# Kernel tuning notes

Measured on AMD Instinct MI355X. Metric: run time of the kernel, lower is better.

The kernel has to match this reference:

```python
import jax, jax.numpy as jnp
import numpy as np

B = 2048      # batchsize from init_kwargs
TAU = 0.5     # temperature from init_kwargs
EPS = 1e-8    # torch CosineSimilarity eps


def _neg_idx(b):
    # For each row i of the (2B,2B) similarity matrix, the columns that are
    # negatives: everything except the diagonal (i) and the positive partner
    # ((i+B) mod 2B). Matches torch mask 1-(eye(k=B)+eye(k=-B)+eye()).
    n = 2 * b
    rows = np.arange(n)
    partner = (rows + b) % n
    cols = np.tile(np.arange(n), (n, 1))
    mask = (cols != rows[:, None]) & (cols != partner[:, None])
    return cols[mask].reshape(n, n - 2)


NEG_IDX = jnp.asarray(_neg_idx(B))  # (2B, 2B-2), int


def setup_inputs() -> dict:
    key = jax.random.key(0)
    k1, k2 = jax.random.split(key)
    D = 1024
    return {
        "z_orig": jax.random.normal(k1, (B, D), dtype=jnp.float32),
        "z_augment": jax.random.normal(k2, (B, D), dtype=jnp.float32),
    }


def reference(z_orig, z_augment):
    n = 2 * B
    z = jnp.concatenate([z_augment, z_orig], axis=0)            # (2B, D)
    norms = jnp.linalg.norm(z, axis=-1, keepdims=True)
    zn = z / jnp.maximum(norms, EPS)
    sim = zn @ zn.T                                             # (2B, 2B) cosine sims
    idx = jnp.arange(n)
    pos = sim[idx, (idx + B) % n]                               # (2B,) positive pairs
    neg = jnp.take_along_axis(sim, NEG_IDX, axis=1)             # (2B, 2B-2)
    logits = jnp.concatenate([pos[:, None], neg], axis=1) / TAU # (2B, 2B-1)
    # CrossEntropy with label 0, reduction='sum':
    loss = jnp.sum(jax.nn.logsumexp(logits, axis=1) - logits[:, 0])
    return loss / n
```

## Files before the change

kernel.cpp:

```cpp
#include <hip/hip_runtime.h>
#include <hip/hip_bf16.h>
#include <math.h>


#define BB   2048
#define N2   4096
#define DIM  1024
#define TAUI 2.0f
#define EPSN 1e-8f

#define BM  128
#define BN  128
#define BKK 64
#define NP  64
#define NBLK 528

typedef __attribute__((ext_vector_type(4))) float f32x4;
typedef __attribute__((ext_vector_type(8))) short s16x8;

__device__ __forceinline__ void gll16(const void* g, void* l) {
    __builtin_amdgcn_global_load_lds(
        (const __attribute__((address_space(1))) void*)g,
        (__attribute__((address_space(3))) void*)l, 16, 0, 0);
}

__global__ __launch_bounds__(256) void k_prep(const float* __restrict__ zO,
                                              const float* __restrict__ zA,
                                              __hip_bfloat16* __restrict__ zb) {
    int row = blockIdx.x;
    const float* zr = (row < BB) ? (zA + (size_t)row * DIM)
                                 : (zO + (size_t)(row - BB) * DIM);
    int t = threadIdx.x;
    float4 v = *(const float4*)(zr + t * 4);
    float s = v.x * v.x + v.y * v.y + v.z * v.z + v.w * v.w;
    for (int m = 1; m < 64; m <<= 1) s += __shfl_xor(s, m);
    __shared__ float wsum[4];
    __shared__ float inv_s;
    int wv = t >> 6, ln = t & 63;
    if (ln == 0) wsum[wv] = s;
    __syncthreads();
    if (t == 0)
        inv_s = 1.0f / fmaxf(sqrtf(wsum[0] + wsum[1] + wsum[2] + wsum[3]), EPSN);
    __syncthreads();
    float inv = inv_s;
    __hip_bfloat16 h0 = __float2bfloat16(v.x * inv);
    __hip_bfloat16 h1 = __float2bfloat16(v.y * inv);
    __hip_bfloat16 h2 = __float2bfloat16(v.z * inv);
    __hip_bfloat16 h3 = __float2bfloat16(v.w * inv);
    ushort4 o;
    o.x = *(unsigned short*)&h0;
    o.y = *(unsigned short*)&h1;
    o.z = *(unsigned short*)&h2;
    o.w = *(unsigned short*)&h3;
    ((ushort4*)zb)[(size_t)row * (DIM / 4) + t] = o;
}

__global__ __launch_bounds__(256) void k_lse(const __hip_bfloat16* __restrict__ zb,
                                             float* __restrict__ pm,
                                             float* __restrict__ pl,
                                             float* __restrict__ pos) {
    __shared__ __hip_bfloat16 As[BM * BKK];
    __shared__ __hip_bfloat16 Bs[BN * BKK];

    int lin = blockIdx.x;
    int ti = (int)((65.0f - sqrtf(4225.0f - 8.0f * (float)lin)) * 0.5f);
    while ((ti + 1) * (65 - (ti + 1)) / 2 <= lin) ti++;
    while (ti * (65 - ti) / 2 > lin) ti--;
    int tj = ti + (lin - ti * (65 - ti) / 2);

    int ibase = ti * BM, jbase = tj * BN;
    int tid = threadIdx.x;
    int w = tid >> 6, l = tid & 63;
    int wr = w >> 1, wc = w & 1;
    int rl = l & 15, kg = l >> 4;

    const __hip_bfloat16* Ag = zb + (size_t)ibase * DIM;
    const __hip_bfloat16* Bg = zb + (size_t)jbase * DIM;

    f32x4 acc[4][4];
#pragma unroll
    for (int m = 0; m < 4; m++)
#pragma unroll
        for (int n = 0; n < 4; n++) acc[m][n] = (f32x4){0.f, 0.f, 0.f, 0.f};

    int srow = l >> 3;
    int scol = (l & 7) * 8;

    for (int kt = 0; kt < DIM; kt += BKK) {
        __syncthreads();
#pragma unroll
        for (int s4 = 0; s4 < 4; s4++) {
            int s = w * 4 + s4;
            int grow = 8 * s + srow;
            gll16(Ag + (size_t)grow * DIM + kt + scol, &As[s * 512]);
            gll16(Bg + (size_t)grow * DIM + kt + scol, &Bs[s * 512]);
        }
        __syncthreads();

#pragma unroll
        for (int kk = 0; kk < 2; kk++) {
            s16x8 a[4], b[4];
#pragma unroll
            for (int m = 0; m < 4; m++)
                a[m] = *(const s16x8*)&As[(wr * 64 + m * 16 + rl) * BKK + kk * 32 + kg * 8];
#pragma unroll
            for (int n = 0; n < 4; n++)
                b[n] = *(const s16x8*)&Bs[(wc * 64 + n * 16 + rl) * BKK + kk * 32 + kg * 8];
#pragma unroll
            for (int m = 0; m < 4; m++)
#pragma unroll
                for (int n = 0; n < 4; n++)
                    acc[m][n] = __builtin_amdgcn_mfma_f32_16x16x32_bf16(
                        a[m], b[n], acc[m][n], 0, 0, 0);
        }
    }

    int rowbase = ibase + wr * 64;
    int colbase = jbase + wc * 64;
    int slot = tj * 2 + wc;
#pragma unroll
    for (int m = 0; m < 4; m++) {
#pragma unroll
        for (int r = 0; r < 4; r++) {
            int ig = rowbase + m * 16 + kg * 4 + r;
            int pp = (ig + BB) & (N2 - 1);
            float v[4];
            float rmax = -1e30f;
#pragma unroll
            for (int n = 0; n < 4; n++) {
                int jg = colbase + n * 16 + rl;
                float val = acc[m][n][r] * TAUI;
                if (jg == pp) { pos[ig] = val; pos[jg] = val; }
                if (jg == ig) val = -1e30f;
                v[n] = val;
                rmax = fmaxf(rmax, val);
            }
#pragma unroll
            for (int mk = 1; mk < 16; mk <<= 1)
                rmax = fmaxf(rmax, __shfl_xor(rmax, mk));
            float ssum = 0.f;
#pragma unroll
            for (int n = 0; n < 4; n++) ssum += __expf(v[n] - rmax);
#pragma unroll
            for (int mk = 1; mk < 16; mk <<= 1) ssum += __shfl_xor(ssum, mk);
            if (rl == 0) {
                pm[(size_t)ig * NP + slot] = rmax;
                pl[(size_t)ig * NP + slot] = ssum;
            }
        }
    }

    if (ti != tj) {
        int slot2 = ti * 2 + wr;
#pragma unroll
        for (int n = 0; n < 4; n++) {
            float cmax = -1e30f;
#pragma unroll
            for (int m = 0; m < 4; m++)
#pragma unroll
                for (int r = 0; r < 4; r++)
                    cmax = fmaxf(cmax, acc[m][n][r] * TAUI);
            cmax = fmaxf(cmax, __shfl_xor(cmax, 16));
            cmax = fmaxf(cmax, __shfl_xor(cmax, 32));
            float cs = 0.f;
#pragma unroll
            for (int m = 0; m < 4; m++)
#pragma unroll
                for (int r = 0; r < 4; r++)
                    cs += __expf(acc[m][n][r] * TAUI - cmax);
            cs += __shfl_xor(cs, 16);
            cs += __shfl_xor(cs, 32);
            if (l < 16) {
                int jg = colbase + n * 16 + rl;
                pm[(size_t)jg * NP + slot2] = cmax;
                pl[(size_t)jg * NP + slot2] = cs;
            }
        }
    }
}

__global__ __launch_bounds__(256) void k_combine(const float* __restrict__ pm,
                                                 const float* __restrict__ pl,
                                                 const float* __restrict__ pos,
                                                 float* __restrict__ out) {
    int row = blockIdx.x * 256 + threadIdx.x;
    const float* P = pm + (size_t)row * NP;
    const float* L = pl + (size_t)row * NP;
    float M = -1e30f;
#pragma unroll
    for (int c = 0; c < NP; c++) M = fmaxf(M, P[c]);
    float S = 0.f;
#pragma unroll
    for (int c = 0; c < NP; c++) S += L[c] * __expf(P[c] - M);
    float v = M + __logf(S) - pos[row];
    for (int mk = 1; mk < 64; mk <<= 1) v += __shfl_xor(v, mk);
    __shared__ float wsum[4];
    int wv = threadIdx.x >> 6, ln = threadIdx.x & 63;
    if (ln == 0) wsum[wv] = v;
    __syncthreads();
    if (threadIdx.x == 0)
        atomicAdd(out, (wsum[0] + wsum[1] + wsum[2] + wsum[3]) * (1.0f / (float)N2));
}

extern "C" void kernel_launch(void* const* d_in, const int* in_sizes, int n_in,
                              void* d_out, int out_size, void* d_ws, size_t ws_size,
                              hipStream_t stream) {
    const float* zO = (const float*)d_in[0];
    const float* zA = (const float*)d_in[1];
    float* out = (float*)d_out;

    __hip_bfloat16* zb = (__hip_bfloat16*)d_ws;
    float* pm  = (float*)((char*)d_ws + (size_t)N2 * DIM * 2);
    float* pl  = pm + (size_t)N2 * NP;
    float* pos = pl + (size_t)N2 * NP;

    hipMemsetAsync(out, 0, sizeof(float), stream);
    k_prep<<<N2, 256, 0, stream>>>(zO, zA, zb);
    k_lse<<<NBLK, 256, 0, stream>>>(zb, pm, pl, pos);
    k_combine<<<N2 / 256, 256, 0, stream>>>(pm, pl, pos, out);
}
```

Before: 133.8 us.

## Double-buffer LDS tiles in the similarity GEMM to overlap loads with MFMA

Turns the shared-memory A/B tiles in the fused GEMM+logsumexp kernel into two buffers. The next K-slice is prefetched with global_load_lds while MFMAs run on the current one, and explicit vmcnt/lgkmcnt waits plus raw barriers order the work. The goal is to hide global load latency that the old load-sync-compute loop exposed. In exchange it doubles LDS use, which may lower occupancy, and it depends on a hand-counted vmcnt value.

```diff
diff --git a/kernel.cpp b/kernel.cpp
--- a/kernel.cpp
+++ b/kernel.cpp
@@ -12,6 +12,7 @@
 #define BM  128
 #define BN  128
 #define BKK 64
+#define NK  (DIM / BKK)
 #define NP  64
 #define NBLK 528
 
@@ -59,8 +60,8 @@
                                              float* __restrict__ pm,
                                              float* __restrict__ pl,
                                              float* __restrict__ pos) {
-    __shared__ __hip_bfloat16 As[BM * BKK];
-    __shared__ __hip_bfloat16 Bs[BN * BKK];
+    __shared__ __hip_bfloat16 As[2][BM * BKK];
+    __shared__ __hip_bfloat16 Bs[2][BN * BKK];
 
     int lin = blockIdx.x;
     int ti = (int)((65.0f - sqrtf(4225.0f - 8.0f * (float)lin)) * 0.5f);
@@ -86,26 +87,37 @@
     int srow = l >> 3;
     int scol = (l & 7) * 8;
 
-    for (int kt = 0; kt < DIM; kt += BKK) {
-        __syncthreads();
+    auto stage = [&](int buf, int kt) {
 #pragma unroll
         for (int s4 = 0; s4 < 4; s4++) {
             int s = w * 4 + s4;
             int grow = 8 * s + srow;
-            gll16(Ag + (size_t)grow * DIM + kt + scol, &As[s * 512]);
-            gll16(Bg + (size_t)grow * DIM + kt + scol, &Bs[s * 512]);
-        }
-        __syncthreads();
+            gll16(Ag + (size_t)grow * DIM + kt + scol, &As[buf][s * 512]);
+            gll16(Bg + (size_t)grow * DIM + kt + scol, &Bs[buf][s * 512]);
+        }
+    };
+
+    stage(0, 0);
+    int cur = 0;
+    for (int kt = 0; kt < NK; kt++) {
+        if (kt + 1 < NK) {
+            stage(cur ^ 1, (kt + 1) * BKK);
+            asm volatile("s_waitcnt vmcnt(8)" ::: "memory");
+        } else {
+            asm volatile("s_waitcnt vmcnt(0)" ::: "memory");
+        }
+        __builtin_amdgcn_sched_barrier(0);
+        __builtin_amdgcn_s_barrier();
 
 #pragma unroll
         for (int kk = 0; kk < 2; kk++) {
             s16x8 a[4], b[4];
 #pragma unroll
             for (int m = 0; m < 4; m++)
-                a[m] = *(const s16x8*)&As[(wr * 64 + m * 16 + rl) * BKK + kk * 32 + kg * 8];
+                a[m] = *(const s16x8*)&As[cur][(wr * 64 + m * 16 + rl) * BKK + kk * 32 + kg * 8];
 #pragma unroll
             for (int n = 0; n < 4; n++)
-                b[n] = *(const s16x8*)&Bs[(wc * 64 + n * 16 + rl) * BKK + kk * 32 + kg * 8];
+                b[n] = *(const s16x8*)&Bs[cur][(wc * 64 + n * 16 + rl) * BKK + kk * 32 + kg * 8];
 #pragma unroll
             for (int m = 0; m < 4; m++)
 #pragma unroll
@@ -113,6 +125,11 @@
                     acc[m][n] = __builtin_amdgcn_mfma_f32_16x16x32_bf16(
                         a[m], b[n], acc[m][n], 0, 0, 0);
         }
+
+        asm volatile("s_waitcnt lgkmcnt(0)" ::: "memory");
+        __builtin_amdgcn_sched_barrier(0);
+        __builtin_amdgcn_s_barrier();
+        cur ^= 1;
     }
 
     int rowbase = ibase + wr * 64;
```

Result: no change. 133.8 us (+0.0%).

## Swizzle LDS tiles, use 8 waves per GEMM tile, streamline prep and combine

Applied to the files above, without the earlier changes.

The LSE GEMM kernel now runs 512 threads (a 2x4 wave grid, each wave computing 64x32) instead of 256, which halves the per-wave accumulators. It also applies an XOR swizzle to the LDS chunk layout during global-to-LDS loads and MFMA operand reads, to avoid LDS bank conflicts. The partial-result slot count grows to 128, and the buffer is zeroed with a memset so unused slots are harmless. The prep kernel now handles one row per wave with no block barriers, and the combine kernel uses vectorized loads with an online max/sum. The costs are an extra memset and twice the partial storage.

```diff
diff --git a/kernel.cpp b/kernel.cpp
--- a/kernel.cpp
+++ b/kernel.cpp
@@ -12,8 +12,9 @@
 #define BM  128
 #define BN  128
 #define BKK 64
-#define NP  64
-#define NBLK 528
+#define NK  (DIM / BKK)
+#define NP  128
+#define NTRI 528
 
 typedef __attribute__((ext_vector_type(4))) float f32x4;
 typedef __attribute__((ext_vector_type(8))) short s16x8;
@@ -27,35 +28,36 @@
 __global__ __launch_bounds__(256) void k_prep(const float* __restrict__ zO,
                                               const float* __restrict__ zA,
                                               __hip_bfloat16* __restrict__ zb) {
-    int row = blockIdx.x;
+    int row = (blockIdx.x * 256 + threadIdx.x) >> 6;
+    int lane = threadIdx.x & 63;
     const float* zr = (row < BB) ? (zA + (size_t)row * DIM)
                                  : (zO + (size_t)(row - BB) * DIM);
-    int t = threadIdx.x;
-    float4 v = *(const float4*)(zr + t * 4);
-    float s = v.x * v.x + v.y * v.y + v.z * v.z + v.w * v.w;
+    float4 v[4];
+    float s = 0.f;
+#pragma unroll
+    for (int q = 0; q < 4; q++) {
+        v[q] = *(const float4*)(zr + q * 256 + lane * 4);
+        s += v[q].x * v[q].x + v[q].y * v[q].y + v[q].z * v[q].z + v[q].w * v[q].w;
+    }
+#pragma unroll
     for (int m = 1; m < 64; m <<= 1) s += __shfl_xor(s, m);
-    __shared__ float wsum[4];
-    __shared__ float inv_s;
-    int wv = t >> 6, ln = t & 63;
-    if (ln == 0) wsum[wv] = s;
-    __syncthreads();
-    if (t == 0)
-        inv_s = 1.0f / fmaxf(sqrtf(wsum[0] + wsum[1] + wsum[2] + wsum[3]), EPSN);
-    __syncthreads();
-    float inv = inv_s;
-    __hip_bfloat16 h0 = __float2bfloat16(v.x * inv);
-    __hip_bfloat16 h1 = __float2bfloat16(v.y * inv);
-    __hip_bfloat16 h2 = __float2bfloat16(v.z * inv);
-    __hip_bfloat16 h3 = __float2bfloat16(v.w * inv);
-    ushort4 o;
-    o.x = *(unsigned short*)&h0;
-    o.y = *(unsigned short*)&h1;
-    o.z = *(unsigned short*)&h2;
-    o.w = *(unsigned short*)&h3;
-    ((ushort4*)zb)[(size_t)row * (DIM / 4) + t] = o;
-}
-
-__global__ __launch_bounds__(256) void k_lse(const __hip_bfloat16* __restrict__ zb,
+    float inv = 1.0f / fmaxf(sqrtf(s), EPSN);
+#pragma unroll
+    for (int q = 0; q < 4; q++) {
+        __hip_bfloat16 h0 = __float2bfloat16(v[q].x * inv);
+        __hip_bfloat16 h1 = __float2bfloat16(v[q].y * inv);
+        __hip_bfloat16 h2 = __float2bfloat16(v[q].z * inv);
+        __hip_bfloat16 h3 = __float2bfloat16(v[q].w * inv);
+        ushort4 o;
+        o.x = *(unsigned short*)&h0;
+        o.y = *(unsigned short*)&h1;
+        o.z = *(unsigned short*)&h2;
+        o.w = *(unsigned short*)&h3;
+        ((ushort4*)zb)[(size_t)row * 256 + q * 64 + lane] = o;
+    }
+}
+
+__global__ __launch_bounds__(512) void k_lse(const __hip_bfloat16* __restrict__ zb,
                                              float* __restrict__ pm,
                                              float* __restrict__ pl,
                                              float* __restrict__ pos) {
@@ -71,26 +73,26 @@
     int ibase = ti * BM, jbase = tj * BN;
     int tid = threadIdx.x;
     int w = tid >> 6, l = tid & 63;
-    int wr = w >> 1, wc = w & 1;
+    int wr = w >> 2, wc = w & 3;
     int rl = l & 15, kg = l >> 4;
+    int cx = l & 7;
+    int srow = l >> 3;
+    int scol = ((cx ^ srow) * 8);
 
     const __hip_bfloat16* Ag = zb + (size_t)ibase * DIM;
     const __hip_bfloat16* Bg = zb + (size_t)jbase * DIM;
 
-    f32x4 acc[4][4];
+    f32x4 acc[4][2];
 #pragma unroll
     for (int m = 0; m < 4; m++)
 #pragma unroll
-        for (int n = 0; n < 4; n++) acc[m][n] = (f32x4){0.f, 0.f, 0.f, 0.f};
-
-    int srow = l >> 3;
-    int scol = (l & 7) * 8;
+        for (int n = 0; n < 2; n++) acc[m][n] = (f32x4){0.f, 0.f, 0.f, 0.f};
 
     for (int kt = 0; kt < DIM; kt += BKK) {
         __syncthreads();
 #pragma unroll
-        for (int s4 = 0; s4 < 4; s4++) {
-            int s = w * 4 + s4;
+        for (int s4 = 0; s4 < 2; s4++) {
+            int s = w * 2 + s4;
             int grow = 8 * s + srow;
             gll16(Ag + (size_t)grow * DIM + kt + scol, &As[s * 512]);
             gll16(Bg + (size_t)grow * DIM + kt + scol, &Bs[s * 512]);
@@ -99,35 +101,36 @@
 
 #pragma unroll
         for (int kk = 0; kk < 2; kk++) {
-            s16x8 a[4], b[4];
-#pragma unroll
-            for (int m = 0; m < 4; m++)
-                a[m] = *(const s16x8*)&As[(wr * 64 + m * 16 + rl) * BKK + kk * 32 + kg * 8];
-#pragma unroll
-            for (int n = 0; n < 4; n++)
-                b[n] = *(const s16x8*)&Bs[(wc * 64 + n * 16 + rl) * BKK + kk * 32 + kg * 8];
-#pragma unroll
-            for (int m = 0; m < 4; m++)
-#pragma unroll
-                for (int n = 0; n < 4; n++)
+            s16x8 a[4], b[2];
+            int ch = (((kk * 4 + kg) ^ (rl & 7)) * 8);
+#pragma unroll
+            for (int m = 0; m < 4; m++)
+                a[m] = *(const s16x8*)&As[(wr * 64 + m * 16 + rl) * BKK + ch];
+#pragma unroll
+            for (int n = 0; n < 2; n++)
+                b[n] = *(const s16x8*)&Bs[(wc * 32 + n * 16 + rl) * BKK + ch];
+#pragma unroll
+            for (int m = 0; m < 4; m++)
+#pragma unroll
+                for (int n = 0; n < 2; n++)
                     acc[m][n] = __builtin_amdgcn_mfma_f32_16x16x32_bf16(
                         a[m], b[n], acc[m][n], 0, 0, 0);
         }
     }
 
     int rowbase = ibase + wr * 64;
-    int colbase = jbase + wc * 64;
-    int slot = tj * 2 + wc;
+    int colbase = jbase + wc * 32;
+    int slot = tj * 4 + wc;
 #pragma unroll
     for (int m = 0; m < 4; m++) {
 #pragma unroll
         for (int r = 0; r < 4; r++) {
             int ig = rowbase + m * 16 + kg * 4 + r;
             int pp = (ig + BB) & (N2 - 1);
-            float v[4];
+            float v[2];
             float rmax = -1e30f;
 #pragma unroll
-            for (int n = 0; n < 4; n++) {
+            for (int n = 0; n < 2; n++) {
                 int jg = colbase + n * 16 + rl;
                 float val = acc[m][n][r] * TAUI;
                 if (jg == pp) { pos[ig] = val; pos[jg] = val; }
@@ -140,7 +143,7 @@
                 rmax = fmaxf(rmax, __shfl_xor(rmax, mk));
             float ssum = 0.f;
 #pragma unroll
-            for (int n = 0; n < 4; n++) ssum += __expf(v[n] - rmax);
+            for (int n = 0; n < 2; n++) ssum += __expf(v[n] - rmax);
 #pragma unroll
             for (int mk = 1; mk < 16; mk <<= 1) ssum += __shfl_xor(ssum, mk);
             if (rl == 0) {
@@ -153,7 +156,7 @@
     if (ti != tj) {
         int slot2 = ti * 2 + wr;
 #pragma unroll
-        for (int n = 0; n < 4; n++) {
+        for (int n = 0; n < 2; n++) {
             float cmax = -1e30f;
 #pragma unroll
             for (int m = 0; m < 4; m++)
@@ -184,15 +187,20 @@
                                                  const float* __restrict__ pos,
                                                  float* __restrict__ out) {
     int row = blockIdx.x * 256 + threadIdx.x;
-    const float* P = pm + (size_t)row * NP;
-    const float* L = pl + (size_t)row * NP;
-    float M = -1e30f;
-#pragma unroll
-    for (int c = 0; c < NP; c++) M = fmaxf(M, P[c]);
-    float S = 0.f;
-#pragma unroll
-    for (int c = 0; c < NP; c++) S += L[c] * __expf(P[c] - M);
+    const float4* P4 = (const float4*)(pm + (size_t)row * NP);
+    const float4* L4 = (const float4*)(pl + (size_t)row * NP);
+    float M = -1e30f, S = 0.f;
+#pragma unroll
+    for (int c = 0; c < NP / 4; c++) {
+        float4 p = P4[c], q = L4[c];
+        float nm = fmaxf(M, fmaxf(fmaxf(p.x, p.y), fmaxf(p.z, p.w)));
+        S = S * __expf(M - nm)
+          + q.x * __expf(p.x - nm) + q.y * __expf(p.y - nm)
+          + q.z * __expf(p.z - nm) + q.w * __expf(p.w - nm);
+        M = nm;
+    }
     float v = M + __logf(S) - pos[row];
+#pragma unroll
     for (int mk = 1; mk < 64; mk <<= 1) v += __shfl_xor(v, mk);
     __shared__ float wsum[4];
     int wv = threadIdx.x >> 6, ln = threadIdx.x & 63;
@@ -215,7 +223,8 @@
     float* pos = pl + (size_t)N2 * NP;
 
     hipMemsetAsync(out, 0, sizeof(float), stream);
-    k_prep<<<N2, 256, 0, stream>>>(zO, zA, zb);
-    k_lse<<<NBLK, 256, 0, stream>>>(zb, pm, pl, pos);
+    hipMemsetAsync(pm, 0, (size_t)N2 * NP * 2 * sizeof(float), stream);
+    k_prep<<<N2 / 4, 256, 0, stream>>>(zO, zA, zb);
+    k_lse<<<NTRI, 512, 0, stream>>>(zb, pm, pl, pos);
     k_combine<<<N2 / 256, 256, 0, stream>>>(pm, pl, pos, out);
 }
```

After: 125.9 us. 5.9% less time.
